# Kernel optimization log

Hardware: AMD Instinct MI355X
Metric: run time of the kernel (lower is better)

## Reference

```python
import jax, jax.numpy as jnp
import numpy as np

NUM_CLASS = 32000

def setup_inputs() -> dict:
    key = jax.random.key(0)
    x = jax.random.randint(key, (8, 1024), 0, NUM_CLASS, dtype=jnp.int64 if jax.config.jax_enable_x64 else jnp.int32)
    return {"x": x}

def reference(x) -> jnp.ndarray:
    # Faithful vectorized form of the nested-loop one-hot build:
    # out[i, j, x[i, j]] = 1, all else 0. Shape [B, S, NUM_CLASS], float32.
    return jax.nn.one_hot(x, NUM_CLASS, dtype=jnp.float32)
```

## Files before the change

kernel.cpp:

```cpp
#include <hip/hip_runtime.h>


#define NUM_CLASS 32000
#define BLOCK 256

__global__ __launch_bounds__(BLOCK) void onehot_kernel(const int* __restrict__ x,
                                                       float* __restrict__ out) {
    const int row = blockIdx.x;
    const int target = x[row];
    float4* __restrict__ orow = (float4*)(out + (size_t)row * NUM_CLASS);

    const int nvec = NUM_CLASS / 4;
    for (int k = threadIdx.x; k < nvec; k += BLOCK) {
        const int c = k * 4;
        float4 v;
        v.x = (c + 0 == target) ? 1.0f : 0.0f;
        v.y = (c + 1 == target) ? 1.0f : 0.0f;
        v.z = (c + 2 == target) ? 1.0f : 0.0f;
        v.w = (c + 3 == target) ? 1.0f : 0.0f;
        orow[k] = v;
    }
}

extern "C" void kernel_launch(void* const* d_in, const int* in_sizes, int n_in,
                              void* d_out, int out_size, void* d_ws, size_t ws_size,
                              hipStream_t stream) {
    const int* x = (const int*)d_in[0];
    float* out = (float*)d_out;
    const int rows = in_sizes[0];
    onehot_kernel<<<rows, BLOCK, 0, stream>>>(x, out);
}
```

Measured before the change: 1.013 ms.

## Split one-hot into grid-stride zero fill plus scatter of ones

Replaces the per-row compare-and-select kernel with two kernels: a grid-stride float4 zero fill over the whole output, then a small kernel that writes 1.0 at each row's target index. This removes the per-element compare work and lets the fill use a fixed 8192-block grid. The cost is a second kernel launch and a dependency between the two launches.

```diff
diff --git a/kernel.cpp b/kernel.cpp
--- a/kernel.cpp
+++ b/kernel.cpp
@@ -4,21 +4,22 @@
 #define NUM_CLASS 32000
 #define BLOCK 256
 
-__global__ __launch_bounds__(BLOCK) void onehot_kernel(const int* __restrict__ x,
-                                                       float* __restrict__ out) {
-    const int row = blockIdx.x;
-    const int target = x[row];
-    float4* __restrict__ orow = (float4*)(out + (size_t)row * NUM_CLASS);
+__global__ __launch_bounds__(BLOCK) void zero_fill_kernel(float4* __restrict__ out,
+                                                          int nvec) {
+    const int stride = gridDim.x * BLOCK;
+    const float4 z = make_float4(0.f, 0.f, 0.f, 0.f);
+    for (int k = blockIdx.x * BLOCK + threadIdx.x; k < nvec; k += stride) {
+        out[k] = z;
+    }
+}
 
-    const int nvec = NUM_CLASS / 4;
-    for (int k = threadIdx.x; k < nvec; k += BLOCK) {
-        const int c = k * 4;
-        float4 v;
-        v.x = (c + 0 == target) ? 1.0f : 0.0f;
-        v.y = (c + 1 == target) ? 1.0f : 0.0f;
-        v.z = (c + 2 == target) ? 1.0f : 0.0f;
-        v.w = (c + 3 == target) ? 1.0f : 0.0f;
-        orow[k] = v;
+__global__ __launch_bounds__(BLOCK) void scatter_ones_kernel(const int* __restrict__ x,
+                                                             float* __restrict__ out,
+                                                             int rows) {
+    const int row = blockIdx.x * BLOCK + threadIdx.x;
+    if (row < rows) {
+        const int t = x[row];
+        out[(size_t)row * NUM_CLASS + t] = 1.0f;
     }
 }
 
@@ -28,5 +29,8 @@
     const int* x = (const int*)d_in[0];
     float* out = (float*)d_out;
     const int rows = in_sizes[0];
-    onehot_kernel<<<rows, BLOCK, 0, stream>>>(x, out);
+    const int nvec = out_size / 4;
+
+    zero_fill_kernel<<<8192, BLOCK, 0, stream>>>((float4*)out, nvec);
+    scatter_ones_kernel<<<(rows + BLOCK - 1) / BLOCK, BLOCK, 0, stream>>>(x, out, rows);
 }
```

New measurement: 982.0 us. -3.0%, faster.
